# Kernel optimization log

Measured on AMD Instinct MI355X. Metric: run time of the kernel, lower is better.

## Reference

```python
import jax, jax.numpy as jnp
import numpy as np

EMBED_DIM = 768
NUM_HEADS = 12
HEAD_DIM = EMBED_DIM // NUM_HEADS
MLP_HIDDEN = int(EMBED_DIM * 4.0)
LN_EPS = 1e-5


def setup_inputs() -> dict:
    key = jax.random.key(0)
    ks = jax.random.split(key, 8)
    C, H = EMBED_DIM, MLP_HIDDEN
    s = 0.02
    return {
        "x": jax.random.normal(ks[0], (2, 2048, C), dtype=jnp.float32),
        "ln1_g": jnp.ones((C,), jnp.float32),
        "ln1_b": jnp.zeros((C,), jnp.float32),
        "qkv_w": jax.random.normal(ks[1], (3 * C, C), jnp.float32) * s,
        "proj_w": jax.random.normal(ks[2], (C, C), jnp.float32) * s,
        "proj_b": jnp.zeros((C,), jnp.float32),
        "ln2_g": jnp.ones((C,), jnp.float32),
        "ln2_b": jnp.zeros((C,), jnp.float32),
        "fc1_w": jax.random.normal(ks[3], (H, C), jnp.float32) * s,
        "fc1_b": jnp.zeros((H,), jnp.float32),
        "fc2_w": jax.random.normal(ks[4], (C, H), jnp.float32) * s,
        "fc2_b": jnp.zeros((C,), jnp.float32),
    }


def _layernorm(x, g, b):
    mu = jnp.mean(x, axis=-1, keepdims=True)
    var = jnp.mean(jnp.square(x - mu), axis=-1, keepdims=True)
    return (x - mu) * jax.lax.rsqrt(var + LN_EPS) * g + b


def reference(x, ln1_g, ln1_b, qkv_w, proj_w, proj_b, ln2_g, ln2_b,
              fc1_w, fc1_b, fc2_w, fc2_b):
    B, N, C = x.shape
    Hh, Dh = NUM_HEADS, HEAD_DIM
    scale = Dh ** -0.5

    # --- attention branch (pre-norm) ---
    h = _layernorm(x, ln1_g, ln1_b)
    qkv = h @ qkv_w.T                                   # [B,N,3C]
    qkv = qkv.reshape(B, N, 3, Hh, Dh)
    q = qkv[:, :, 0].transpose(0, 2, 1, 3)              # [B,H,N,D]
    k = qkv[:, :, 1].transpose(0, 2, 1, 3)
    v = qkv[:, :, 2].transpose(0, 2, 1, 3)
    attn = jnp.einsum('bhnd,bhmd->bhnm', q, k) * scale  # [B,H,N,N]
    attn = jax.nn.softmax(attn, axis=-1)
    o = jnp.einsum('bhnm,bhmd->bhnd', attn, v)          # [B,H,N,D]
    o = o.transpose(0, 2, 1, 3).reshape(B, N, C)
    x = x + o @ proj_w.T + proj_b

    # --- MLP branch (pre-norm), exact GELU like nn.GELU ---
    h = _layernorm(x, ln2_g, ln2_b)
    h = jax.nn.gelu(h @ fc1_w.T + fc1_b, approximate=False)
    x = x + h @ fc2_w.T + fc2_b
    return x
```

## Files before the change

### kernel.cpp

```cpp
#include <hip/hip_runtime.h>
#include <hip/hip_bf16.h>
#include <cstdint>
#include <math.h>


typedef __bf16 bf16_t;
typedef bf16_t bf16x4 __attribute__((ext_vector_type(4)));
typedef bf16_t bf16x8 __attribute__((ext_vector_type(8)));
typedef float floatx4 __attribute__((ext_vector_type(4)));

#define AS1 __attribute__((address_space(1)))
#define AS3 __attribute__((address_space(3)))

__device__ __forceinline__ void async_load16(const void* g, void* l) {
  const AS1 unsigned int* gp =
      reinterpret_cast<const AS1 unsigned int*>(reinterpret_cast<uintptr_t>(g));
  AS3 unsigned int* lp = reinterpret_cast<AS3 unsigned int*>(
      static_cast<unsigned int>(reinterpret_cast<uintptr_t>(l)));
  __builtin_amdgcn_global_load_lds(gp, lp, 16, 0, 0);
}

__device__ __forceinline__ bf16x8 lds_read8(const bf16_t* p) {
  return *reinterpret_cast<const bf16x8*>(p);
}

__global__ __launch_bounds__(256) void cvt_k(const float* __restrict__ in,
                                             bf16_t* __restrict__ out, int n4) {
  const int i = blockIdx.x * 256 + threadIdx.x;
  if (i < n4) {
    const float4 v = reinterpret_cast<const float4*>(in)[i];
    bf16x4 o;
    o[0] = (bf16_t)v.x; o[1] = (bf16_t)v.y; o[2] = (bf16_t)v.z; o[3] = (bf16_t)v.w;
    reinterpret_cast<bf16x4*>(out)[i] = o;
  }
}

__global__ __launch_bounds__(256) void cvt_all_k(
    const float* __restrict__ s0, const float* __restrict__ s1,
    const float* __restrict__ s2, const float* __restrict__ s3,
    bf16_t* __restrict__ d0, bf16_t* __restrict__ d1, bf16_t* __restrict__ d2,
    bf16_t* __restrict__ d3) {
  int i = blockIdx.x * 256 + threadIdx.x;
  const float* src;
  bf16_t* dst;
  if (i < 442368) { src = s0; dst = d0; }
  else if (i < 589824) { src = s1; dst = d1; i -= 442368; }
  else if (i < 1179648) { src = s2; dst = d2; i -= 589824; }
  else if (i < 1769472) { src = s3; dst = d3; i -= 1179648; }
  else return;
  const float4 v = reinterpret_cast<const float4*>(src)[i];
  bf16x4 o;
  o[0] = (bf16_t)v.x; o[1] = (bf16_t)v.y; o[2] = (bf16_t)v.z; o[3] = (bf16_t)v.w;
  reinterpret_cast<bf16x4*>(dst)[i] = o;
}

template <int INIT>
__global__ __launch_bounds__(256) void ln_k(const float* __restrict__ x,
                                            const float* __restrict__ g,
                                            const float* __restrict__ b,
                                            bf16_t* __restrict__ out,
                                            const float* __restrict__ b2,
                                            float* __restrict__ oinit) {
  const int row = blockIdx.x;
  const int tid = threadIdx.x;
  const float* xr = x + (long)row * 768;
  float v[3];
#pragma unroll
  for (int e = 0; e < 3; e++) v[e] = xr[tid + e * 256];
  float s = v[0] + v[1] + v[2];
  float ss = v[0] * v[0] + v[1] * v[1] + v[2] * v[2];
#pragma unroll
  for (int off = 32; off >= 1; off >>= 1) {
    s += __shfl_down(s, off, 64);
    ss += __shfl_down(ss, off, 64);
  }
  __shared__ float red[8];
  __shared__ float stat[2];
  const int wv = tid >> 6;
  if ((tid & 63) == 0) { red[wv] = s; red[4 + wv] = ss; }
  __syncthreads();
  if (tid == 0) {
    float S = red[0] + red[1] + red[2] + red[3];
    float SS = red[4] + red[5] + red[6] + red[7];
    float mu = S * (1.0f / 768.0f);
    float var = SS * (1.0f / 768.0f) - mu * mu;
    stat[0] = mu;
    stat[1] = rsqrtf(var + 1e-5f);
  }
  __syncthreads();
  const float mu = stat[0], rs = stat[1];
#pragma unroll
  for (int e = 0; e < 3; e++) {
    int c = tid + e * 256;
    out[(long)row * 768 + c] = (bf16_t)((v[e] - mu) * rs * g[c] + b[c]);
    if constexpr (INIT == 1) oinit[(long)row * 768 + c] = v[e] + b2[c];
  }
}

template <int MODE>
__global__ __launch_bounds__(256, 2) void gemm_k(
    const bf16_t* __restrict__ A, const bf16_t* __restrict__ Bt, int lda,
    int ldb, int keff, int Nld, const float* __restrict__ bias,
    bf16_t* __restrict__ out_bf, bf16_t* __restrict__ q_out,
    bf16_t* __restrict__ k_out, bf16_t* __restrict__ vt_out) {
  constexpr int BK = 32;
  __shared__ __align__(16) bf16_t As[3][128 * BK];
  __shared__ __align__(16) bf16_t Bs[3][128 * BK];

  const int tid = threadIdx.x;
  const int w = tid >> 6;
  const int lane = tid & 63;
  const int quad = lane >> 4;
  const int lid = lane & 15;
  const int wr = (w >> 1) * 64;
  const int wc = (w & 1) * 64;
  const int mBase = blockIdx.y * 128;
  const int nBase = blockIdx.x * 128;

  const int ldsRowSub = lane >> 2;
  const int kblk = (lane & 3) ^ (ldsRowSub & 3) ^ ((ldsRowSub >> 2) & 3);
  const int rq0 = (quad ^ (lid & 3) ^ ((lid >> 2) & 3)) * 8;
  const int c0 = w * 2, c1 = w * 2 + 1;
  const int rowA0 = c0 * 16 + ldsRowSub, rowA1 = c1 * 16 + ldsRowSub;

  const bf16_t* Ag = A + (long)mBase * lda;
  const bf16_t* Bg = Bt + (long)nBase * ldb;

  floatx4 acc[4][4];
#pragma unroll
  for (int i = 0; i < 4; i++)
#pragma unroll
    for (int j = 0; j < 4; j++) acc[i][j] = (floatx4){0.f, 0.f, 0.f, 0.f};

  auto stage = [&](int b, int k0) {
    async_load16(Ag + (long)rowA0 * lda + k0 + kblk * 8, &As[b][c0 * 512]);
    async_load16(Ag + (long)rowA1 * lda + k0 + kblk * 8, &As[b][c1 * 512]);
    async_load16(Bg + (long)rowA0 * ldb + k0 + kblk * 8, &Bs[b][c0 * 512]);
    async_load16(Bg + (long)rowA1 * ldb + k0 + kblk * 8, &Bs[b][c1 * 512]);
  };

  const int iters = keff / BK;
  stage(0, 0);
  stage(1, BK);

  int cur = 0;
  for (int it = 0; it < iters; it++) {
    if (it + 1 < iters)
      asm volatile("s_waitcnt vmcnt(4) lgkmcnt(0)" ::: "memory");
    else
      asm volatile("s_waitcnt vmcnt(0) lgkmcnt(0)" ::: "memory");
    __builtin_amdgcn_s_barrier();
    if (it + 2 < iters) {
      int nb = cur + 2; if (nb >= 3) nb -= 3;
      stage(nb, (it + 2) * BK);
    }

    bf16x8 af[4], bfv[4];
#pragma unroll
    for (int i = 0; i < 4; i++)
      af[i] = lds_read8(&As[cur][(wr + i * 16 + lid) * BK + rq0]);
#pragma unroll
    for (int j = 0; j < 4; j++)
      bfv[j] = lds_read8(&Bs[cur][(wc + j * 16 + lid) * BK + rq0]);
#pragma unroll
    for (int i = 0; i < 4; i++)
#pragma unroll
      for (int j = 0; j < 4; j++)
        acc[i][j] = __builtin_amdgcn_mfma_f32_16x16x32_bf16(af[i], bfv[j],
                                                            acc[i][j], 0, 0, 0);
    cur = (cur == 2) ? 0 : cur + 1;
  }

#pragma unroll
  for (int i = 0; i < 4; i++) {
    const int mRow = mBase + wr + i * 16 + quad * 4;
#pragma unroll
    for (int j = 0; j < 4; j++) {
      const int n = nBase + wc + j * 16 + lid;
      if constexpr (MODE == 0) {
        const int which = n / 768;
        const int rem = n - which * 768;
        const int head = rem >> 6;
        const int d = rem & 63;
        const int b = mRow >> 11;
        const int t = mRow & 2047;
        const int bh = b * 12 + head;
        if (which == 2) {
          bf16x4 pk;
#pragma unroll
          for (int r = 0; r < 4; r++) pk[r] = (bf16_t)acc[i][j][r];
          const long off = ((long)bh * 64 + d) * 2048 + t;
          *reinterpret_cast<bf16x4*>(&vt_out[off]) = pk;
        } else if (which == 0) {
#pragma unroll
          for (int r = 0; r < 4; r++)
            q_out[((long)bh * 2048 + t + r) * 64 + d] =
                (bf16_t)(acc[i][j][r] * 0.125f);
        } else {
#pragma unroll
          for (int r = 0; r < 4; r++)
            k_out[((long)bh * 2048 + t + r) * 64 + d] = (bf16_t)acc[i][j][r];
        }
      } else {
        const float bv = bias[n];
#pragma unroll
        for (int r = 0; r < 4; r++) {
          float v = acc[i][j][r] + bv;
          float ge = 0.5f * v * (1.0f + erff(v * 0.70710678118654752f));
          out_bf[(long)(mRow + r) * Nld + n] = (bf16_t)ge;
        }
      }
    }
  }
}

template <int MODE>
__global__ __launch_bounds__(256, 4) void gemm64_k(
    const bf16_t* __restrict__ A, const bf16_t* __restrict__ Bt, int lda,
    int ldb, int keff, int Nld, const float* __restrict__ bias,
    const float* __restrict__ resid_f, float* __restrict__ out_f) {
  constexpr int BK = 32;
  __shared__ __align__(16) bf16_t As[3][128 * BK];
  __shared__ __align__(16) bf16_t Bs[3][64 * BK];

  const int tid = threadIdx.x;
  const int w = tid >> 6;
  const int lane = tid & 63;
  const int quad = lane >> 4;
  const int lid = lane & 15;
  const int mBase = blockIdx.x * 128;
  const int nBase = blockIdx.y * 64;
  const int kOff = blockIdx.z * keff;

  const int ldsRowSub = lane >> 2;
  const int kblk = (lane & 3) ^ (ldsRowSub & 3) ^ ((ldsRowSub >> 2) & 3);
  const int rq0 = (quad ^ (lid & 3) ^ ((lid >> 2) & 3)) * 8;
  const int rowA0 = w * 16 + ldsRowSub;
  const int rowA1 = (w + 4) * 16 + ldsRowSub;

  const bf16_t* Ag = A + (long)mBase * lda + kOff;
  const bf16_t* Bg = Bt + (long)nBase * ldb + kOff;

  floatx4 acc[2][4];
#pragma unroll
  for (int i = 0; i < 2; i++)
#pragma unroll
    for (int j = 0; j < 4; j++) acc[i][j] = (floatx4){0.f, 0.f, 0.f, 0.f};

  auto stage = [&](int b, int k0) {
    async_load16(Ag + (long)rowA0 * lda + k0 + kblk * 8, &As[b][w * 512]);
    async_load16(Ag + (long)rowA1 * lda + k0 + kblk * 8, &As[b][(w + 4) * 512]);
    async_load16(Bg + (long)rowA0 * ldb + k0 + kblk * 8, &Bs[b][w * 512]);
  };

  const int iters = keff / BK;
  stage(0, 0);
  stage(1, BK);

  int cur = 0;
  for (int it = 0; it < iters; it++) {
    if (it + 1 < iters)
      asm volatile("s_waitcnt vmcnt(3) lgkmcnt(0)" ::: "memory");
    else
      asm volatile("s_waitcnt vmcnt(0) lgkmcnt(0)" ::: "memory");
    __builtin_amdgcn_s_barrier();
    if (it + 2 < iters) {
      int nb = cur + 2; if (nb >= 3) nb -= 3;
      stage(nb, (it + 2) * BK);
    }

    bf16x8 af[2], bfv[4];
#pragma unroll
    for (int i = 0; i < 2; i++)
      af[i] = lds_read8(&As[cur][(w * 32 + i * 16 + lid) * BK + rq0]);
#pragma unroll
    for (int j = 0; j < 4; j++)
      bfv[j] = lds_read8(&Bs[cur][(j * 16 + lid) * BK + rq0]);
#pragma unroll
    for (int i = 0; i < 2; i++)
#pragma unroll
      for (int j = 0; j < 4; j++)
        acc[i][j] = __builtin_amdgcn_mfma_f32_16x16x32_bf16(af[i], bfv[j],
                                                            acc[i][j], 0, 0, 0);
    cur = (cur == 2) ? 0 : cur + 1;
  }

#pragma unroll
  for (int i = 0; i < 2; i++) {
    const int mRow = mBase + w * 32 + i * 16 + quad * 4;
#pragma unroll
    for (int j = 0; j < 4; j++) {
      const int n = nBase + j * 16 + lid;
      if constexpr (MODE == 1) {
        const float bv = bias[n];
#pragma unroll
        for (int r = 0; r < 4; r++) {
          const long off = (long)(mRow + r) * Nld + n;
          out_f[off] = resid_f[off] + acc[i][j][r] + bv;
        }
      } else {
#pragma unroll
        for (int r = 0; r < 4; r++) {
          const long off = (long)(mRow + r) * Nld + n;
          unsafeAtomicAdd(&out_f[off], acc[i][j][r]);
        }
      }
    }
  }
}

__global__ __launch_bounds__(512, 1) void flash_k(const bf16_t* __restrict__ q,
                                                  const bf16_t* __restrict__ kk,
                                                  const bf16_t* __restrict__ vt,
                                                  bf16_t* __restrict__ U,
                                                  float* __restrict__ lbuf) {
  constexpr int SK = 64, D = 64;
  __shared__ __align__(16) bf16_t Ks[2][SK * D];
  __shared__ __align__(16) bf16_t Vs[2][D * SK];

  const int tid = threadIdx.x;
  const int w = tid >> 6;
  const int lane = tid & 63;
  const int quad = lane >> 4;
  const int lid = lane & 15;
  const int bh = blockIdx.y;
  const int half = blockIdx.z;
  const int qBase = blockIdx.x * 128;

  const bf16_t* qg = q + ((long)bh * 2048 + qBase) * D;
  const bf16_t* kg = kk + ((long)bh * 2048 + half * 1024) * D;
  const bf16_t* vg = vt + (long)bh * D * 2048 + half * 1024;

  bf16x8 aq[2];
#pragma unroll
  for (int k2 = 0; k2 < 2; k2++)
    aq[k2] = *reinterpret_cast<const bf16x8*>(qg + (w * 16 + lid) * D +
                                              k2 * 32 + quad * 8);

  const int srow = lane >> 3;
  const int sdb = (lane & 7) ^ srow;
  const int rsw = lid & 7;

  async_load16(kg + (long)(w * 8 + srow) * D + sdb * 8, &Ks[0][w * 512]);
  async_load16(vg + (long)(w * 8 + srow) * 2048 + sdb * 8, &Vs[0][w * 512]);

  float lsum = 0.f;
  floatx4 oacc[4];
#pragma unroll
  for (int jo = 0; jo < 4; jo++) oacc[jo] = (floatx4){0.f, 0.f, 0.f, 0.f};

  int cur = 0;
  for (int kci = 0; kci < 16; kci++) {
    __syncthreads();
    if (kci + 1 < 16) {
      const int kc = (kci + 1) * 64;
      const int nb = cur ^ 1;
      async_load16(kg + (long)(kc + w * 8 + srow) * D + sdb * 8, &Ks[nb][w * 512]);
      async_load16(vg + (long)(w * 8 + srow) * 2048 + kc + sdb * 8, &Vs[nb][w * 512]);
    }

    floatx4 sacc[4];
#pragma unroll
    for (int jm = 0; jm < 4; jm++) sacc[jm] = (floatx4){0.f, 0.f, 0.f, 0.f};
#pragma unroll
    for (int k2 = 0; k2 < 2; k2++) {
#pragma unroll
      for (int jm = 0; jm < 4; jm++) {
        const bf16x8 ak = lds_read8(
            &Ks[cur][(jm * 16 + lid) * D + (((k2 * 4 + quad) ^ rsw) * 8)]);
        sacc[jm] =
            __builtin_amdgcn_mfma_f32_16x16x32_bf16(ak, aq[k2], sacc[jm], 0, 0, 0);
      }
    }

    bf16x8 ap[2];
#pragma unroll
    for (int k2 = 0; k2 < 2; k2++) {
      uint32_t pk[2][2];
#pragma unroll
      for (int j = 0; j < 2; j++) {
        const int jm = k2 * 2 + j;
        const float p0 = exp2f(fmaf(sacc[jm][0], 1.44269504f, -11.5415603f));
        const float p1 = exp2f(fmaf(sacc[jm][1], 1.44269504f, -11.5415603f));
        const float p2 = exp2f(fmaf(sacc[jm][2], 1.44269504f, -11.5415603f));
        const float p3 = exp2f(fmaf(sacc[jm][3], 1.44269504f, -11.5415603f));
        lsum += ((p0 + p1) + p2) + p3;
        asm("v_cvt_pk_bf16_f32 %0, %1, %2" : "=v"(pk[j][0]) : "v"(p0), "v"(p1));
        asm("v_cvt_pk_bf16_f32 %0, %1, %2" : "=v"(pk[j][1]) : "v"(p2), "v"(p3));
      }
      asm("v_permlane32_swap_b32 %0, %1" : "+v"(pk[0][0]), "+v"(pk[1][0]));
      asm("v_permlane16_swap_b32 %0, %1" : "+v"(pk[0][0]), "+v"(pk[1][0]));
      asm("v_permlane32_swap_b32 %0, %1" : "+v"(pk[0][1]), "+v"(pk[1][1]));
      asm("v_permlane16_swap_b32 %0, %1" : "+v"(pk[0][1]), "+v"(pk[1][1]));
      union { uint32_t u[4]; bf16x8 v; } au;
      au.u[0] = pk[0][0];
      au.u[1] = pk[0][1];
      au.u[2] = pk[1][0];
      au.u[3] = pk[1][1];
      ap[k2] = au.v;
    }

#pragma unroll
    for (int k2 = 0; k2 < 2; k2++) {
#pragma unroll
      for (int jo = 0; jo < 4; jo++) {
        const bf16x8 bv = lds_read8(
            &Vs[cur][(jo * 16 + lid) * SK + (((k2 * 4 + quad) ^ rsw) * 8)]);
        oacc[jo] =
            __builtin_amdgcn_mfma_f32_16x16x32_bf16(ap[k2], bv, oacc[jo], 0, 0, 0);
      }
    }
    cur ^= 1;
  }

  lsum += __shfl_xor(lsum, 16, 64);
  lsum += __shfl_xor(lsum, 32, 64);

  const long lrow = ((long)half * 24 + bh) * 2048 + qBase + w * 16;
  if (quad == 0) lbuf[lrow + lid] = lsum;

  bf16_t* Ub = U + (((long)half * 24 + bh) * 2048 + qBase) * D;
#pragma unroll
  for (int jo = 0; jo < 4; jo++) {
#pragma unroll
    for (int r = 0; r < 4; r++) {
      const int t = w * 16 + quad * 4 + r;
      Ub[(long)t * D + jo * 16 + lid] = (bf16_t)oacc[jo][r];
    }
  }
}

__global__ __launch_bounds__(256) void combine_k(const bf16_t* __restrict__ U,
                                                 const float* __restrict__ lbuf,
                                                 bf16_t* __restrict__ o) {
  const int idx = blockIdx.x * 256 + threadIdx.x;
  const int bh = idx >> 17;
  const int rem = idx & 131071;
  const int t = rem >> 6;
  const int d = rem & 63;
  const float l0 = lbuf[bh * 2048 + t];
  const float l1 = lbuf[(24 + bh) * 2048 + t];
  const float u = (float)U[idx] + (float)U[3145728 + idx];
  const int b = bh / 12;
  const int head = bh - b * 12;
  o[((long)b * 2048 + t) * 768 + head * 64 + d] = (bf16_t)(u / (l0 + l1));
}

extern "C" void kernel_launch(void* const* d_in, const int* in_sizes, int n_in,
                              void* d_out, int out_size, void* d_ws,
                              size_t ws_size, hipStream_t stream) {
  (void)in_sizes; (void)n_in; (void)out_size;
  const float* x = (const float*)d_in[0];
  const float* ln1_g = (const float*)d_in[1];
  const float* ln1_b = (const float*)d_in[2];
  const float* qkv_w = (const float*)d_in[3];
  const float* proj_w = (const float*)d_in[4];
  const float* proj_b = (const float*)d_in[5];
  const float* ln2_g = (const float*)d_in[6];
  const float* ln2_b = (const float*)d_in[7];
  const float* fc1_w = (const float*)d_in[8];
  const float* fc1_b = (const float*)d_in[9];
  const float* fc2_w = (const float*)d_in[10];
  const float* fc2_b = (const float*)d_in[11];
  float* out = (float*)d_out;
  char* ws = (char*)d_ws;

  const bool big = ws_size >= (size_t)64487424;

  if (big) {
    bf16_t* wqkv = (bf16_t*)(ws + 0);
    bf16_t* wproj = (bf16_t*)(ws + 3538944);
    bf16_t* wfc1 = (bf16_t*)(ws + 4718592);
    bf16_t* wfc2 = (bf16_t*)(ws + 9437184);
    bf16_t* h1 = (bf16_t*)(ws + 14155776);
    bf16_t* ob = h1;
    bf16_t* qb = (bf16_t*)(ws + 20447232);
    bf16_t* kb = (bf16_t*)(ws + 26738688);
    bf16_t* vtb = (bf16_t*)(ws + 33030144);
    bf16_t* Ubuf = (bf16_t*)(ws + 39321600);
    float* lbuf = (float*)(ws + 51904512);
    float* x1 = (float*)(ws + 20447232);
    bf16_t* h2 = (bf16_t*)(ws + 33030144);
    bf16_t* hg = (bf16_t*)(ws + 39321600);

    cvt_all_k<<<6912, 256, 0, stream>>>(qkv_w, proj_w, fc1_w, fc2_w, wqkv,
                                        wproj, wfc1, wfc2);
    ln_k<0><<<4096, 256, 0, stream>>>(x, ln1_g, ln1_b, h1, nullptr, nullptr);
    gemm_k<0><<<dim3(18, 32), 256, 0, stream>>>(h1, wqkv, 768, 768, 768, 2304,
                                                nullptr, nullptr, qb, kb, vtb);
    flash_k<<<dim3(16, 24, 2), 512, 0, stream>>>(qb, kb, vtb, Ubuf, lbuf);
    combine_k<<<12288, 256, 0, stream>>>(Ubuf, lbuf, ob);
    gemm64_k<1><<<dim3(32, 12), 256, 0, stream>>>(ob, wproj, 768, 768, 768, 768,
                                                  proj_b, x, x1);
    ln_k<1><<<4096, 256, 0, stream>>>(x1, ln2_g, ln2_b, h2, fc2_b, out);
    gemm_k<2><<<dim3(24, 32), 256, 0, stream>>>(h2, wfc1, 768, 768, 768, 3072,
                                                fc1_b, hg, nullptr, nullptr,
                                                nullptr);
    gemm64_k<6><<<dim3(32, 12, 2), 256, 0, stream>>>(hg, wfc2, 3072, 3072, 1536,
                                                     768, nullptr, nullptr, out);
  } else {
    bf16_t* wqkv = (bf16_t*)(ws + 0);
    bf16_t* wproj = (bf16_t*)(ws + 3538944);
    bf16_t* h1 = (bf16_t*)(ws + 4718592);
    bf16_t* ob = h1;
    bf16_t* qb = (bf16_t*)(ws + 11010048);
    bf16_t* kb = (bf16_t*)(ws + 17301504);
    bf16_t* vtb = (bf16_t*)(ws + 23592960);
    float* x1 = (float*)(ws + 11010048);
    bf16_t* h2 = (bf16_t*)(ws + 23592960);
    bf16_t* wfc1 = (bf16_t*)(ws + 0);
    bf16_t* wfc2 = (bf16_t*)(ws + 4718592);
    bf16_t* hg = (bf16_t*)(ws + 29884416);
    bf16_t* Ubuf = (bf16_t*)(ws + 29884416);
    float* lbuf = (float*)(ws + 42467328);

    cvt_k<<<1728, 256, 0, stream>>>(qkv_w, wqkv, 442368);
    cvt_k<<<576, 256, 0, stream>>>(proj_w, wproj, 147456);
    ln_k<0><<<4096, 256, 0, stream>>>(x, ln1_g, ln1_b, h1, nullptr, nullptr);
    gemm_k<0><<<dim3(18, 32), 256, 0, stream>>>(h1, wqkv, 768, 768, 768, 2304,
                                                nullptr, nullptr, qb, kb, vtb);
    flash_k<<<dim3(16, 24, 2), 512, 0, stream>>>(qb, kb, vtb, Ubuf, lbuf);
    combine_k<<<12288, 256, 0, stream>>>(Ubuf, lbuf, ob);
    gemm64_k<1><<<dim3(32, 12), 256, 0, stream>>>(ob, wproj, 768, 768, 768, 768,
                                                  proj_b, x, x1);
    cvt_k<<<2304, 256, 0, stream>>>(fc1_w, wfc1, 589824);
    cvt_k<<<2304, 256, 0, stream>>>(fc2_w, wfc2, 589824);
    ln_k<1><<<4096, 256, 0, stream>>>(x1, ln2_g, ln2_b, h2, fc2_b, out);
    for (int h = 0; h < 2; h++) {
      gemm_k<2><<<dim3(12, 32), 256, 0, stream>>>(
          h2, wfc1 + (long)h * 1536 * 768, 768, 768, 768, 1536,
          fc1_b + h * 1536, hg, nullptr, nullptr, nullptr);
      gemm64_k<6><<<dim3(32, 12), 256, 0, stream>>>(hg, wfc2 + h * 1536, 1536,
                                                    3072, 1536, 768, nullptr,
                                                    nullptr, out);
    }
  }
}
```

Before: 284.8 us.

## Replace 128x64 GEMM kernel with 128x128 tile kernel for proj and fc2

Removes the separate 128x64-tile gemm64_k kernel and routes the output projection and fc2 GEMMs through the 128x128-tile gemm_k, which gains residual-add (MODE 3) and atomic split-K (MODE 4) epilogues plus a blockIdx.z K offset. Grid axes are swapped so blockIdx.x walks M rows, changing block scheduling order and L2 reuse of the weight tiles. Larger tiles give more reuse per load, but the proj/fc2 grids halve (192 or 384 blocks) and gemm_k has a lower occupancy bound (2 vs 4), so there is less parallelism on a large-CU GPU.

New measurement: 272.2 us. 4.4% less time.

```diff
diff --git a/kernel.cpp b/kernel.cpp
--- a/kernel.cpp
+++ b/kernel.cpp
@@ -102,7 +102,8 @@
     const bf16_t* __restrict__ A, const bf16_t* __restrict__ Bt, int lda,
     int ldb, int keff, int Nld, const float* __restrict__ bias,
     bf16_t* __restrict__ out_bf, bf16_t* __restrict__ q_out,
-    bf16_t* __restrict__ k_out, bf16_t* __restrict__ vt_out) {
+    bf16_t* __restrict__ k_out, bf16_t* __restrict__ vt_out,
+    const float* __restrict__ resid_f, float* __restrict__ out_f) {
   constexpr int BK = 32;
   __shared__ __align__(16) bf16_t As[3][128 * BK];
   __shared__ __align__(16) bf16_t Bs[3][128 * BK];
@@ -114,8 +115,9 @@
   const int lid = lane & 15;
   const int wr = (w >> 1) * 64;
   const int wc = (w & 1) * 64;
-  const int mBase = blockIdx.y * 128;
-  const int nBase = blockIdx.x * 128;
+  const int mBase = blockIdx.x * 128;
+  const int nBase = blockIdx.y * 128;
+  const int kOff = blockIdx.z * keff;
 
   const int ldsRowSub = lane >> 2;
   const int kblk = (lane & 3) ^ (ldsRowSub & 3) ^ ((ldsRowSub >> 2) & 3);
@@ -123,8 +125,8 @@
   const int c0 = w * 2, c1 = w * 2 + 1;
   const int rowA0 = c0 * 16 + ldsRowSub, rowA1 = c1 * 16 + ldsRowSub;
 
-  const bf16_t* Ag = A + (long)mBase * lda;
-  const bf16_t* Bg = Bt + (long)nBase * ldb;
+  const bf16_t* Ag = A + (long)mBase * lda + kOff;
+  const bf16_t* Bg = Bt + (long)nBase * ldb + kOff;
 
   floatx4 acc[4][4];
 #pragma unroll
@@ -201,7 +203,7 @@
           for (int r = 0; r < 4; r++)
             k_out[((long)bh * 2048 + t + r) * 64 + d] = (bf16_t)acc[i][j][r];
         }
-      } else {
+      } else if constexpr (MODE == 2) {
         const float bv = bias[n];
 #pragma unroll
         for (int r = 0; r < 4; r++) {
@@ -209,89 +211,7 @@
           float ge = 0.5f * v * (1.0f + erff(v * 0.70710678118654752f));
           out_bf[(long)(mRow + r) * Nld + n] = (bf16_t)ge;
         }
-      }
-    }
-  }
-}
-
-template <int MODE>
-__global__ __launch_bounds__(256, 4) void gemm64_k(
-    const bf16_t* __restrict__ A, const bf16_t* __restrict__ Bt, int lda,
-    int ldb, int keff, int Nld, const float* __restrict__ bias,
-    const float* __restrict__ resid_f, float* __restrict__ out_f) {
-  constexpr int BK = 32;
-  __shared__ __align__(16) bf16_t As[3][128 * BK];
-  __shared__ __align__(16) bf16_t Bs[3][64 * BK];
-
-  const int tid = threadIdx.x;
-  const int w = tid >> 6;
-  const int lane = tid & 63;
-  const int quad = lane >> 4;
-  const int lid = lane & 15;
-  const int mBase = blockIdx.x * 128;
-  const int nBase = blockIdx.y * 64;
-  const int kOff = blockIdx.z * keff;
-
-  const int ldsRowSub = lane >> 2;
-  const int kblk = (lane & 3) ^ (ldsRowSub & 3) ^ ((ldsRowSub >> 2) & 3);
-  const int rq0 = (quad ^ (lid & 3) ^ ((lid >> 2) & 3)) * 8;
-  const int rowA0 = w * 16 + ldsRowSub;
-  const int rowA1 = (w + 4) * 16 + ldsRowSub;
-
-  const bf16_t* Ag = A + (long)mBase * lda + kOff;
-  const bf16_t* Bg = Bt + (long)nBase * ldb + kOff;
-
-  floatx4 acc[2][4];
-#pragma unroll
-  for (int i = 0; i < 2; i++)
-#pragma unroll
-    for (int j = 0; j < 4; j++) acc[i][j] = (floatx4){0.f, 0.f, 0.f, 0.f};
-
-  auto stage = [&](int b, int k0) {
-    async_load16(Ag + (long)rowA0 * lda + k0 + kblk * 8, &As[b][w * 512]);
-    async_load16(Ag + (long)rowA1 * lda + k0 + kblk * 8, &As[b][(w + 4) * 512]);
-    async_load16(Bg + (long)rowA0 * ldb + k0 + kblk * 8, &Bs[b][w * 512]);
-  };
-
-  const int iters = keff / BK;
-  stage(0, 0);
-  stage(1, BK);
-
-  int cur = 0;
-  for (int it = 0; it < iters; it++) {
-    if (it + 1 < iters)
-      asm volatile("s_waitcnt vmcnt(3) lgkmcnt(0)" ::: "memory");
-    else
-      asm volatile("s_waitcnt vmcnt(0) lgkmcnt(0)" ::: "memory");
-    __builtin_amdgcn_s_barrier();
-    if (it + 2 < iters) {
-      int nb = cur + 2; if (nb >= 3) nb -= 3;
-      stage(nb, (it + 2) * BK);
-    }
-
-    bf16x8 af[2], bfv[4];
-#pragma unroll
-    for (int i = 0; i < 2; i++)
-      af[i] = lds_read8(&As[cur][(w * 32 + i * 16 + lid) * BK + rq0]);
-#pragma unroll
-    for (int j = 0; j < 4; j++)
-      bfv[j] = lds_read8(&Bs[cur][(j * 16 + lid) * BK + rq0]);
-#pragma unroll
-    for (int i = 0; i < 2; i++)
-#pragma unroll
-      for (int j = 0; j < 4; j++)
-        acc[i][j] = __builtin_amdgcn_mfma_f32_16x16x32_bf16(af[i], bfv[j],
-                                                            acc[i][j], 0, 0, 0);
-    cur = (cur == 2) ? 0 : cur + 1;
-  }
-
-#pragma unroll
-  for (int i = 0; i < 2; i++) {
-    const int mRow = mBase + w * 32 + i * 16 + quad * 4;
-#pragma unroll
-    for (int j = 0; j < 4; j++) {
-      const int n = nBase + j * 16 + lid;
-      if constexpr (MODE == 1) {
+      } else if constexpr (MODE == 3) {
         const float bv = bias[n];
 #pragma unroll
         for (int r = 0; r < 4; r++) {
@@ -486,18 +406,22 @@
     cvt_all_k<<<6912, 256, 0, stream>>>(qkv_w, proj_w, fc1_w, fc2_w, wqkv,
                                         wproj, wfc1, wfc2);
     ln_k<0><<<4096, 256, 0, stream>>>(x, ln1_g, ln1_b, h1, nullptr, nullptr);
-    gemm_k<0><<<dim3(18, 32), 256, 0, stream>>>(h1, wqkv, 768, 768, 768, 2304,
-                                                nullptr, nullptr, qb, kb, vtb);
+    gemm_k<0><<<dim3(32, 18), 256, 0, stream>>>(h1, wqkv, 768, 768, 768, 2304,
+                                                nullptr, nullptr, qb, kb, vtb,
+                                                nullptr, nullptr);
     flash_k<<<dim3(16, 24, 2), 512, 0, stream>>>(qb, kb, vtb, Ubuf, lbuf);
     combine_k<<<12288, 256, 0, stream>>>(Ubuf, lbuf, ob);
-    gemm64_k<1><<<dim3(32, 12), 256, 0, stream>>>(ob, wproj, 768, 768, 768, 768,
-                                                  proj_b, x, x1);
+    gemm_k<3><<<dim3(32, 6), 256, 0, stream>>>(ob, wproj, 768, 768, 768, 768,
+                                               proj_b, nullptr, nullptr,
+                                               nullptr, nullptr, x, x1);
     ln_k<1><<<4096, 256, 0, stream>>>(x1, ln2_g, ln2_b, h2, fc2_b, out);
-    gemm_k<2><<<dim3(24, 32), 256, 0, stream>>>(h2, wfc1, 768, 768, 768, 3072,
+    gemm_k<2><<<dim3(32, 24), 256, 0, stream>>>(h2, wfc1, 768, 768, 768, 3072,
                                                 fc1_b, hg, nullptr, nullptr,
-                                                nullptr);
-    gemm64_k<6><<<dim3(32, 12, 2), 256, 0, stream>>>(hg, wfc2, 3072, 3072, 1536,
-                                                     768, nullptr, nullptr, out);
+                                                nullptr, nullptr, nullptr);
+    gemm_k<4><<<dim3(32, 6, 2), 256, 0, stream>>>(hg, wfc2, 3072, 3072, 1536,
+                                                  768, nullptr, nullptr,
+                                                  nullptr, nullptr, nullptr,
+                                                  nullptr, out);
   } else {
     bf16_t* wqkv = (bf16_t*)(ws + 0);
     bf16_t* wproj = (bf16_t*)(ws + 3538944);
@@ -517,22 +441,25 @@
     cvt_k<<<1728, 256, 0, stream>>>(qkv_w, wqkv, 442368);
     cvt_k<<<576, 256, 0, stream>>>(proj_w, wproj, 147456);
     ln_k<0><<<4096, 256, 0, stream>>>(x, ln1_g, ln1_b, h1, nullptr, nullptr);
-    gemm_k<0><<<dim3(18, 32), 256, 0, stream>>>(h1, wqkv, 768, 768, 768, 2304,
-                                                nullptr, nullptr, qb, kb, vtb);
+    gemm_k<0><<<dim3(32, 18), 256, 0, stream>>>(h1, wqkv, 768, 768, 768, 2304,
+                                                nullptr, nullptr, qb, kb, vtb,
+                                                nullptr, nullptr);
     flash_k<<<dim3(16, 24, 2), 512, 0, stream>>>(qb, kb, vtb, Ubuf, lbuf);
     combine_k<<<12288, 256, 0, stream>>>(Ubuf, lbuf, ob);
-    gemm64_k<1><<<dim3(32, 12), 256, 0, stream>>>(ob, wproj, 768, 768, 768, 768,
-                                                  proj_b, x, x1);
+    gemm_k<3><<<dim3(32, 6), 256, 0, stream>>>(ob, wproj, 768, 768, 768, 768,
+                                               proj_b, nullptr, nullptr,
+                                               nullptr, nullptr, x, x1);
     cvt_k<<<2304, 256, 0, stream>>>(fc1_w, wfc1, 589824);
     cvt_k<<<2304, 256, 0, stream>>>(fc2_w, wfc2, 589824);
     ln_k<1><<<4096, 256, 0, stream>>>(x1, ln2_g, ln2_b, h2, fc2_b, out);
     for (int h = 0; h < 2; h++) {
-      gemm_k<2><<<dim3(12, 32), 256, 0, stream>>>(
+      gemm_k<2><<<dim3(32, 12), 256, 0, stream>>>(
           h2, wfc1 + (long)h * 1536 * 768, 768, 768, 768, 1536,
-          fc1_b + h * 1536, hg, nullptr, nullptr, nullptr);
-      gemm64_k<6><<<dim3(32, 12), 256, 0, stream>>>(hg, wfc2 + h * 1536, 1536,
-                                                    3072, 1536, 768, nullptr,
-                                                    nullptr, out);
-    }
-  }
-}
+          fc1_b + h * 1536, hg, nullptr, nullptr, nullptr, nullptr, nullptr);
+      gemm_k<4><<<dim3(32, 6), 256, 0, stream>>>(hg, wfc2 + h * 1536, 1536,
+                                                 3072, 1536, 768, nullptr,
+                                                 nullptr, nullptr, nullptr,
+                                                 nullptr, nullptr, out);
+    }
+  }
+}
```
